# Performance work log

Hardware: AMD Instinct MI355X
Metric: run time of the kernel (lower is better)

The kernel has to match this reference:

```python
import jax, jax.numpy as jnp
import numpy as np
from jax import lax

N_CLS = 3
ALPHA = 2
NMS = True


def _make_level(key, B, A, D, H, W, P, counts):
    k1, k2, k3, k4, k5 = jax.random.split(key, 5)
    C = N_CLS * A
    logit = jax.random.normal(k1, (B, C, D, H, W), dtype=jnp.float32)
    # valid positive coords use d,h,w >= 1 so padded writes to (0,0,0,0) never collide
    a = jax.random.randint(k2, (B, P), 0, A)
    d = jax.random.randint(k3, (B, P), 1, D)
    h = jax.random.randint(k4, (B, P), 1, H)
    w = jax.random.randint(k5, (B, P), 1, W)
    labels = jax.random.randint(jax.random.fold_in(key, 7), (B, P), 0, N_CLS)
    valid = jnp.arange(P)[None, :] < jnp.asarray(counts)[:, None]  # [B,P]
    coord = jnp.stack([a, d, h, w], axis=-1)
    coord = jnp.where(valid[..., None], coord, -1).astype(jnp.int32)
    # ground-truth prob map: -1 = negative, class id (float) at positive voxels
    prob_gt = -jnp.ones((B, A, D, H, W), dtype=jnp.float32)
    cs = jnp.where(valid[..., None], coord, 0)
    b_idx = jnp.arange(B)[:, None]
    vals = jnp.where(valid, labels.astype(jnp.float32), -1.0)
    prob_gt = prob_gt.at[b_idx, cs[..., 0], cs[..., 1], cs[..., 2], cs[..., 3]].set(vals)
    return logit, prob_gt, coord


def setup_inputs() -> dict:
    key = jax.random.key(0)
    kA, kB = jax.random.split(key)
    logit0, prob_gt0, coord0 = _make_level(kA, 4, 3, 64, 64, 64, 128, [128, 64, 32, 0])
    logit1, prob_gt1, coord1 = _make_level(kB, 4, 3, 32, 32, 32, 128, [64, 16, 8, 128])
    weight_cls = jnp.array([1.0, 1.5, 2.0], dtype=jnp.float32)
    return {
        "logit0": logit0, "logit1": logit1,
        "prob_gt0": prob_gt0, "prob_gt1": prob_gt1,
        "coord0": coord0, "coord1": coord1,
        "weight_cls": weight_cls,
    }


def _level_loss(logit, prob_gt, coord_gt, weight_cls):
    B, C, D, H, W = logit.shape
    A = C // N_CLS
    logit = logit.reshape(B, N_CLS, A, D, H, W)
    logp = jax.nn.log_softmax(logit, axis=1)
    nll = -logp                      # [B,N_cls,A,D,H,W]
    prob = jnp.exp(logp)
    nll_neg = nll[:, 0]              # [B,A,D,H,W]
    prob_neg = prob[:, 0]
    negmask = (prob_gt == -1).astype(logit.dtype)
    if NMS:
        mp = lax.reduce_window(nll_neg, -jnp.inf, lax.max,
                               (1, 1, 3, 3, 3), (1, 1, 1, 1, 1),
                               [(0, 0), (0, 0), (1, 1), (1, 1), (1, 1)])
        negmask = negmask * lax.stop_gradient((mp == nll_neg).astype(logit.dtype))
    w_neg = (1.0 - lax.stop_gradient(prob_neg)) ** ALPHA * negmask
    loss_neg = jnp.sum(nll_neg * w_neg)
    count_neg = jnp.sum(w_neg)
    # positives: ragged coord gather, masked instead of per-sample python loop
    valid = coord_gt[:, :, 0] > -1                       # [B,P]
    c = jnp.where(valid[..., None], coord_gt, 0)         # safe coords
    a, d, h, w = c[..., 0], c[..., 1], c[..., 2], c[..., 3]
    b_idx = jnp.arange(B)[:, None]
    cls = prob_gt[b_idx, a, d, h, w].astype(jnp.int32)   # class id at positives
    cls = jnp.where(valid, cls, 0)
    p_t = prob[b_idx, cls, a, d, h, w]
    nll_t = nll[b_idx, cls, a, d, h, w]
    w_pos = ((1.0 - lax.stop_gradient(p_t)) ** ALPHA
             * weight_cls[cls] * valid.astype(logit.dtype))
    loss_pos = jnp.sum(nll_t * w_pos)
    count_pos = jnp.sum(w_pos)
    return loss_pos, loss_neg, count_pos, count_neg


def reference(logit0, logit1, prob_gt0, prob_gt1, coord0, coord1, weight_cls):
    lp0, ln0, cp0, cn0 = _level_loss(logit0, prob_gt0, coord0, weight_cls)
    lp1, ln1, cp1, cn1 = _level_loss(logit1, prob_gt1, coord1, weight_cls)
    return jnp.stack([lp0 + lp1, ln0 + ln1, cp0 + cp1, cn0 + cn1])
```

## Files before the change

### kernel.cpp

```cpp
#include <hip/hip_runtime.h>
#include <math.h>

#define NEG_INF (-INFINITY)

__device__ __forceinline__ float nll3(float l0, float l1, float l2) {
    float m = fmaxf(l0, fmaxf(l1, l2));
    float e0 = __expf(l0 - m);
    float e1 = __expf(l1 - m);
    float e2 = __expf(l2 - m);
    return __logf(e0 + e1 + e2) - (l0 - m);
}

template<int W, int NR, int TD, int D, int H>
__device__ void neg_strip_p2(int uid, int lane,
                             const float* __restrict__ logit,
                             const float* __restrict__ pg,
                             float2* __restrict__ slot) {
    constexpr int LR = W / 4;
    constexpr int NI = NR + 2;
    constexpr int HG = H / NR;
    constexpr int DT = D / TD;
    const int q = lane % LR;
    const int g = lane / LR;

    int t = uid;
    const int hg = t % HG; t /= HG;
    const int dt = t % DT; t /= DT;
    const int ba = t;
    const int a = ba % 3, b = ba / 3;
    const int h0 = hg * NR, d0 = dt * TD;
    const int HW = H * W;

    const long S = (long)D * HW;
    const float* lb  = logit + ((long)b * 9 + a) * S;
    const long  cs   = 3 * S;
    const float* pgb = pg + (long)ba * S;

    const int jrow = h0 - 1 + g;
    const bool hv = (jrow >= 0) && (jrow < H) && (g < NI);
    const int hcl = min(max(jrow, 0), H - 1);
    const int rowoff = hcl * W + 4 * q;
    const int prowoff = (h0 + min(g, NR - 1)) * W + 4 * q;

    float4 A0, A1, A2, B0, B1, B2, C0, C1, C2;
    float4 GA, GB, GC;
    bool vA, vB, vC;

    {
        const float* p = lb + (long)max(d0 - 1, 0) * HW + rowoff;
        A0 = *(const float4*)p;
        A1 = *(const float4*)(p + cs);
        A2 = *(const float4*)(p + 2 * cs);
        vA = (d0 - 1 >= 0);
        const float* p2 = lb + (long)d0 * HW + rowoff;
        B0 = *(const float4*)p2;
        B1 = *(const float4*)(p2 + cs);
        B2 = *(const float4*)(p2 + 2 * cs);
        vB = true;
        GA = make_float4(0.f, 0.f, 0.f, 0.f);
        GB = make_float4(0.f, 0.f, 0.f, 0.f);
    }

    float vm0[4], vm1[4], cc1[4];
#pragma unroll
    for (int i = 0; i < 4; ++i) { vm0[i] = NEG_INF; vm1[i] = NEG_INF; cc1[i] = 0.f; }

    float loss = 0.f, cnt = 0.f;

#pragma unroll
    for (int s = 0; s <= TD + 1; ++s) {
        if (s <= TD - 1) {
            const int pd = d0 + 1 + s;
            const float* p = lb + (long)min(pd, D - 1) * HW + rowoff;
            C0 = *(const float4*)p;
            C1 = *(const float4*)(p + cs);
            C2 = *(const float4*)(p + 2 * cs);
            vC = (pd < D);
            GC = *(const float4*)(pgb + (long)(d0 + s) * HW + prowoff);
        } else {
            vC = false;
            C0 = C1 = C2 = make_float4(0.f, 0.f, 0.f, 0.f);
            GC = make_float4(0.f, 0.f, 0.f, 0.f);
        }

        float nvv[4];
        {
            const bool vv = vA && hv;
            nvv[0] = vv ? nll3(A0.x, A1.x, A2.x) : NEG_INF;
            nvv[1] = vv ? nll3(A0.y, A1.y, A2.y) : NEG_INF;
            nvv[2] = vv ? nll3(A0.z, A1.z, A2.z) : NEG_INF;
            nvv[3] = vv ? nll3(A0.w, A1.w, A2.w) : NEG_INF;
        }

        float le = __shfl(nvv[3], lane - 1);
        float re = __shfl(nvv[0], lane + 1);
        le = (q == 0)      ? NEG_INF : le;
        re = (q == LR - 1) ? NEG_INF : re;
        float rm[4];
        rm[0] = fmaxf(le,     fmaxf(nvv[0], nvv[1]));
        rm[1] = fmaxf(nvv[0], fmaxf(nvv[1], nvv[2]));
        rm[2] = fmaxf(nvv[1], fmaxf(nvv[2], nvv[3]));
        rm[3] = fmaxf(nvv[2], fmaxf(nvv[3], re));

        float rmA[4], rmB[4], ctr[4];
#pragma unroll
        for (int i = 0; i < 4; ++i) {
            rmA[i] = __shfl(rm[i],  lane + LR);
            rmB[i] = __shfl(rm[i],  lane + 2 * LR);
            ctr[i] = __shfl(nvv[i], lane + LR);
        }

        const float pgv[4] = {GA.x, GA.y, GA.z, GA.w};
#pragma unroll
        for (int i = 0; i < 4; ++i) {
            float hw2 = fmaxf(rm[i], fmaxf(rmA[i], rmB[i]));
            if (s >= 2 && g < NR && pgv[i] == -1.0f) {
                float mp = fmaxf(vm0[i], fmaxf(vm1[i], hw2));
                if (mp == cc1[i]) {
                    float pn = __expf(-cc1[i]);
                    float wn = (1.f - pn) * (1.f - pn);
                    loss += cc1[i] * wn;
                    cnt  += wn;
                }
            }
            vm0[i] = vm1[i]; vm1[i] = hw2; cc1[i] = ctr[i];
        }

        GA = GB; GB = GC;
        A0 = B0; A1 = B1; A2 = B2; vA = vB;
        B0 = C0; B1 = C1; B2 = C2; vB = vC;
    }

#pragma unroll
    for (int off = 32; off > 0; off >>= 1) {
        loss += __shfl_down(loss, off);
        cnt  += __shfl_down(cnt, off);
    }
    if (lane == 0) slot[uid] = make_float2(loss, cnt);
}

__device__ void pos_wave8(int sub, int lane,
                          const float* __restrict__ logit,
                          const float* __restrict__ prob_gt,
                          const int* __restrict__ coord,
                          const float* __restrict__ wcls,
                          float2* __restrict__ slot,
                          int D, int H, int W) {
    const int A = 3, P = 128;
    const long S = (long)D * H * W;
    const int i = sub * 64 + lane;
    const int b = i / P;
    const int* c = coord + (long)i * 4;
    const int a = c[0];
    float loss = 0.f, cnt = 0.f;
    if (a > -1) {
        const int d = c[1], h = c[2], w = c[3];
        const long s = ((long)d * H + h) * W + w;
        const int cls = (int)prob_gt[((long)b * A + a) * S + s];
        const float* lp = logit + ((long)b * 3 * A + a) * S + s;
        float l0 = lp[0];
        float l1 = lp[(long)A * S];
        float l2 = lp[2L * A * S];
        float m = fmaxf(l0, fmaxf(l1, l2));
        float e0 = __expf(l0 - m);
        float e1 = __expf(l1 - m);
        float e2 = __expf(l2 - m);
        float lsum = __logf(e0 + e1 + e2);
        float lc = (cls == 0) ? l0 : ((cls == 1) ? l1 : l2);
        float lpc = (lc - m) - lsum;
        float pt = __expf(lpc);
        float wp = (1.f - pt) * (1.f - pt) * wcls[cls];
        loss = (-lpc) * wp;
        cnt = wp;
    }
#pragma unroll
    for (int off = 32; off > 0; off >>= 1) {
        loss += __shfl_down(loss, off);
        cnt  += __shfl_down(cnt, off);
    }
    if (lane == 0) *slot = make_float2(loss, cnt);
}

#define NW0 6144
#define NW1 768
#define NWP 16
#define NUNEG (NW0 + NW1)
#define TOTAL_WAVES (NW0 + NW1 + NWP)

__global__ __launch_bounds__(256)
void mega_kernel(const float* __restrict__ logit0,
                 const float* __restrict__ logit1,
                 const float* __restrict__ pg0,
                 const float* __restrict__ pg1,
                 const int* __restrict__ coord0,
                 const int* __restrict__ coord1,
                 const float* __restrict__ wcls,
                 float2* __restrict__ ws) {
    const int gw = blockIdx.x * 4 + (threadIdx.x >> 6);
    const int lane = threadIdx.x & 63;
    float2* wsneg = ws;
    float2* wspos = ws + NUNEG;
    if (gw < NW0) {
        neg_strip_p2<64, 2, 4, 64, 64>(gw, lane, logit0, pg0, wsneg);
    } else if (gw < NW0 + NW1) {
        neg_strip_p2<32, 4, 4, 32, 32>(gw - NW0, lane, logit1, pg1, wsneg + NW0);
    } else if (gw < NW0 + NW1 + 8) {
        const int sub = gw - NW0 - NW1;
        pos_wave8(sub, lane, logit0, pg0, coord0, wcls, wspos + sub, 64, 64, 64);
    } else {
        const int sub = gw - NW0 - NW1 - 8;
        pos_wave8(sub, lane, logit1, pg1, coord1, wcls, wspos + 8 + sub, 32, 32, 32);
    }
}

__global__ __launch_bounds__(1024)
void final_reduce(const float2* __restrict__ ws, float* __restrict__ out) {
    const float2* wsneg = ws;
    const float2* wspos = ws + NUNEG;
    float ln = 0.f, cn = 0.f, lp = 0.f, cp = 0.f;
    for (int i = threadIdx.x; i < NUNEG; i += 1024) {
        float2 v = wsneg[i]; ln += v.x; cn += v.y;
    }
    if (threadIdx.x < NWP) {
        float2 v = wspos[threadIdx.x]; lp = v.x; cp = v.y;
    }
#pragma unroll
    for (int off = 32; off > 0; off >>= 1) {
        ln += __shfl_down(ln, off); cn += __shfl_down(cn, off);
        lp += __shfl_down(lp, off); cp += __shfl_down(cp, off);
    }
    __shared__ float s[16][4];
    const int wv = threadIdx.x >> 6;
    if ((threadIdx.x & 63) == 0) {
        s[wv][0] = ln; s[wv][1] = cn; s[wv][2] = lp; s[wv][3] = cp;
    }
    __syncthreads();
    if (threadIdx.x == 0) {
        float a = 0.f, b = 0.f, c = 0.f, d = 0.f;
#pragma unroll
        for (int i = 0; i < 16; ++i) {
            a += s[i][0]; b += s[i][1]; c += s[i][2]; d += s[i][3];
        }
        out[0] = c;
        out[1] = a;
        out[2] = d;
        out[3] = b;
    }
}

extern "C" void kernel_launch(void* const* d_in, const int* in_sizes, int n_in,
                              void* d_out, int out_size, void* d_ws, size_t ws_size,
                              hipStream_t stream) {
    const float* logit0   = (const float*)d_in[0];
    const float* logit1   = (const float*)d_in[1];
    const float* prob_gt0 = (const float*)d_in[2];
    const float* prob_gt1 = (const float*)d_in[3];
    const int*   coord0   = (const int*)d_in[4];
    const int*   coord1   = (const int*)d_in[5];
    const float* wcls     = (const float*)d_in[6];
    float* out = (float*)d_out;
    float2* ws = (float2*)d_ws;

    mega_kernel<<<TOTAL_WAVES / 4, 256, 0, stream>>>(
        logit0, logit1, prob_gt0, prob_gt1, coord0, coord1, wcls, ws);
    final_reduce<<<1, 1024, 0, stream>>>(ws, out);
}
```

Measured before the change: 107.7 us.

## Tile negative NMS over whole blocks with LDS-shared NLL and halo reuse

Replaces per-wave 3D max-pool strips with per-block tiles of many H rows. Each block computes NLL once into LDS ring buffers and builds the separable 3x3x3 max from shared row and plane maxima. This cuts the redundant halo loads and NLL recomputation of the small per-wave strips. In exchange it adds LDS traffic, two block barriers per depth step, and an intra-block reduction.

```diff
diff --git a/kernel.cpp b/kernel.cpp
--- a/kernel.cpp
+++ b/kernel.cpp
@@ -11,124 +11,155 @@
     return __logf(e0 + e1 + e2) - (l0 - m);
 }
 
-template<int W, int NR, int TD, int D, int H>
-__device__ void neg_strip_p2(int uid, int lane,
-                             const float* __restrict__ logit,
-                             const float* __restrict__ pg,
-                             float2* __restrict__ slot) {
-    constexpr int LR = W / 4;
-    constexpr int NI = NR + 2;
-    constexpr int HG = H / NR;
-    constexpr int DT = D / TD;
-    const int q = lane % LR;
-    const int g = lane / LR;
-
-    int t = uid;
-    const int hg = t % HG; t /= HG;
-    const int dt = t % DT; t /= DT;
+__device__ __forceinline__ float4 fmax4(float4 a, float4 b) {
+    return make_float4(fmaxf(a.x, b.x), fmaxf(a.y, b.y),
+                       fmaxf(a.z, b.z), fmaxf(a.w, b.w));
+}
+
+template<int W, int HT, int ZT, int D, int H>
+__device__ void neg_block(int ub, int tid,
+                          const float* __restrict__ logit,
+                          const float* __restrict__ pg,
+                          float2* __restrict__ slot,
+                          float* lds, float2* red) {
+    constexpr int LQ = W / 4;
+    constexpr int SR = W + 4;
+    constexpr int SROWS = HT + 2;
+    constexpr int QS = SROWS * LQ;
+    constexpr int HW = H * W;
+    constexpr int ZTI = D / ZT;
+    constexpr int HTI = H / HT;
+    constexpr int NLL_SZ = SROWS * SR;
+    constexpr int HV_OFF = 3 * NLL_SZ;
+    constexpr int HV_SZ = HT * SR;
+
+    int t = ub;
+    const int ht = t % HTI; t /= HTI;
+    const int zt = t % ZTI; t /= ZTI;
     const int ba = t;
     const int a = ba % 3, b = ba / 3;
-    const int h0 = hg * NR, d0 = dt * TD;
-    const int HW = H * W;
+    const int z0 = zt * ZT, h0 = ht * HT;
 
     const long S = (long)D * HW;
+    const long cs = 3 * S;
     const float* lb  = logit + ((long)b * 9 + a) * S;
-    const long  cs   = 3 * S;
     const float* pgb = pg + (long)ba * S;
 
-    const int jrow = h0 - 1 + g;
-    const bool hv = (jrow >= 0) && (jrow < H) && (g < NI);
-    const int hcl = min(max(jrow, 0), H - 1);
-    const int rowoff = hcl * W + 4 * q;
-    const int prowoff = (h0 + min(g, NR - 1)) * W + 4 * q;
-
-    float4 A0, A1, A2, B0, B1, B2, C0, C1, C2;
-    float4 GA, GB, GC;
-    bool vA, vB, vC;
-
-    {
-        const float* p = lb + (long)max(d0 - 1, 0) * HW + rowoff;
-        A0 = *(const float4*)p;
-        A1 = *(const float4*)(p + cs);
-        A2 = *(const float4*)(p + 2 * cs);
-        vA = (d0 - 1 >= 0);
-        const float* p2 = lb + (long)d0 * HW + rowoff;
-        B0 = *(const float4*)p2;
-        B1 = *(const float4*)(p2 + cs);
-        B2 = *(const float4*)(p2 + 2 * cs);
-        vB = true;
-        GA = make_float4(0.f, 0.f, 0.f, 0.f);
-        GB = make_float4(0.f, 0.f, 0.f, 0.f);
-    }
-
-    float vm0[4], vm1[4], cc1[4];
-#pragma unroll
-    for (int i = 0; i < 4; ++i) { vm0[i] = NEG_INF; vm1[i] = NEG_INF; cc1[i] = 0.f; }
+    const int er = tid / LQ;
+    const int q  = tid % LQ;
+    const int lane = tid & 63;
+    const int l_er = er * SR + 4 * q;
+    const int po = (h0 + er) * W + 4 * q;
+
+    int roff[2]; bool rok[2];
+#pragma unroll
+    for (int r = 0; r < 2; ++r) {
+        const int k = tid + 256 * r;
+        const int row = k / LQ, qq = k % LQ;
+        const int h = h0 - 1 + row;
+        rok[r]  = (k < QS) && (h >= 0) && (h < H);
+        roff[r] = min(max(h, 0), H - 1) * W + 4 * qq;
+    }
+
+    float4 rA[2][3] = {}, rB[2][3] = {};
+    float4 pgA = {}, pgB = {};
+    bool pvA, pvB = false;
+
+    auto issue = [&](float4 (&rg)[2][3], int zp) -> bool {
+        const bool pv = (zp >= 0) && (zp < D);
+        if (pv) {
+#pragma unroll
+            for (int r = 0; r < 2; ++r) {
+                if (tid + 256 * r < QS) {
+                    const float* p = lb + (long)zp * HW + roff[r];
+                    rg[r][0] = *(const float4*)p;
+                    rg[r][1] = *(const float4*)(p + cs);
+                    rg[r][2] = *(const float4*)(p + 2 * cs);
+                }
+            }
+        }
+        return pv;
+    };
+
+    pvA = issue(rA, z0 - 1);
 
     float loss = 0.f, cnt = 0.f;
 
 #pragma unroll
-    for (int s = 0; s <= TD + 1; ++s) {
-        if (s <= TD - 1) {
-            const int pd = d0 + 1 + s;
-            const float* p = lb + (long)min(pd, D - 1) * HW + rowoff;
-            C0 = *(const float4*)p;
-            C1 = *(const float4*)(p + cs);
-            C2 = *(const float4*)(p + 2 * cs);
-            vC = (pd < D);
-            GC = *(const float4*)(pgb + (long)(d0 + s) * HW + prowoff);
-        } else {
-            vC = false;
-            C0 = C1 = C2 = make_float4(0.f, 0.f, 0.f, 0.f);
-            GC = make_float4(0.f, 0.f, 0.f, 0.f);
-        }
-
-        float nvv[4];
+    for (int zi = 0; zi <= ZT + 1; ++zi) {
+        const int zc = z0 - 1 + zi;
+        if (zi <= ZT) pvB = issue(rB, zc + 1);
+        if (zi >= 1 && zi <= ZT)
+            pgB = *(const float4*)(pgb + (long)zc * HW + po);
+
         {
-            const bool vv = vA && hv;
-            nvv[0] = vv ? nll3(A0.x, A1.x, A2.x) : NEG_INF;
-            nvv[1] = vv ? nll3(A0.y, A1.y, A2.y) : NEG_INF;
-            nvv[2] = vv ? nll3(A0.z, A1.z, A2.z) : NEG_INF;
-            nvv[3] = vv ? nll3(A0.w, A1.w, A2.w) : NEG_INF;
-        }
-
-        float le = __shfl(nvv[3], lane - 1);
-        float re = __shfl(nvv[0], lane + 1);
-        le = (q == 0)      ? NEG_INF : le;
-        re = (q == LR - 1) ? NEG_INF : re;
-        float rm[4];
-        rm[0] = fmaxf(le,     fmaxf(nvv[0], nvv[1]));
-        rm[1] = fmaxf(nvv[0], fmaxf(nvv[1], nvv[2]));
-        rm[2] = fmaxf(nvv[1], fmaxf(nvv[2], nvv[3]));
-        rm[3] = fmaxf(nvv[2], fmaxf(nvv[3], re));
-
-        float rmA[4], rmB[4], ctr[4];
-#pragma unroll
-        for (int i = 0; i < 4; ++i) {
-            rmA[i] = __shfl(rm[i],  lane + LR);
-            rmB[i] = __shfl(rm[i],  lane + 2 * LR);
-            ctr[i] = __shfl(nvv[i], lane + LR);
-        }
-
-        const float pgv[4] = {GA.x, GA.y, GA.z, GA.w};
-#pragma unroll
-        for (int i = 0; i < 4; ++i) {
-            float hw2 = fmaxf(rm[i], fmaxf(rmA[i], rmB[i]));
-            if (s >= 2 && g < NR && pgv[i] == -1.0f) {
-                float mp = fmaxf(vm0[i], fmaxf(vm1[i], hw2));
-                if (mp == cc1[i]) {
-                    float pn = __expf(-cc1[i]);
+            float* nb = lds + (zi % 3) * NLL_SZ;
+#pragma unroll
+            for (int r = 0; r < 2; ++r) {
+                const int k = tid + 256 * r;
+                if (k < QS) {
+                    const int row = k / LQ, qq = k % LQ;
+                    const bool ok = pvA && rok[r];
+                    float4 n;
+                    n.x = ok ? nll3(rA[r][0].x, rA[r][1].x, rA[r][2].x) : NEG_INF;
+                    n.y = ok ? nll3(rA[r][0].y, rA[r][1].y, rA[r][2].y) : NEG_INF;
+                    n.z = ok ? nll3(rA[r][0].z, rA[r][1].z, rA[r][2].z) : NEG_INF;
+                    n.w = ok ? nll3(rA[r][0].w, rA[r][1].w, rA[r][2].w) : NEG_INF;
+                    *(float4*)(nb + row * SR + 4 * qq) = n;
+                }
+            }
+        }
+        __syncthreads();
+
+        {
+            const float* nb = lds + (zi % 3) * NLL_SZ;
+            float* hb = lds + HV_OFF + (zi % 3) * HV_SZ;
+            float4 v0 = *(const float4*)(nb + l_er);
+            float4 v1 = *(const float4*)(nb + l_er + SR);
+            float4 v2 = *(const float4*)(nb + l_er + 2 * SR);
+            float4 vm = fmax4(v0, fmax4(v1, v2));
+            float le = __shfl(vm.w, lane - 1);
+            float re = __shfl(vm.x, lane + 1);
+            le = (q == 0)      ? NEG_INF : le;
+            re = (q == LQ - 1) ? NEG_INF : re;
+            float4 hv;
+            hv.x = fmaxf(le,   fmaxf(vm.x, vm.y));
+            hv.y = fmaxf(vm.x, fmaxf(vm.y, vm.z));
+            hv.z = fmaxf(vm.y, fmaxf(vm.z, vm.w));
+            hv.w = fmaxf(vm.z, fmaxf(vm.w, re));
+            *(float4*)(hb + l_er) = hv;
+        }
+        __syncthreads();
+
+        if (zi >= 2) {
+            const float* nbm = lds + ((zi - 1) % 3) * NLL_SZ;
+            const float* hb0 = lds + HV_OFF + ((zi - 2) % 3) * HV_SZ;
+            const float* hb1 = lds + HV_OFF + ((zi - 1) % 3) * HV_SZ;
+            const float* hb2 = lds + HV_OFF + (zi % 3) * HV_SZ;
+            float4 nc = *(const float4*)(nbm + l_er + SR);
+            float4 m  = fmax4(*(const float4*)(hb0 + l_er),
+                        fmax4(*(const float4*)(hb1 + l_er),
+                              *(const float4*)(hb2 + l_er)));
+            const float pgv[4] = {pgA.x, pgA.y, pgA.z, pgA.w};
+            const float ncv[4] = {nc.x, nc.y, nc.z, nc.w};
+            const float mv[4]  = {m.x, m.y, m.z, m.w};
+#pragma unroll
+            for (int i = 0; i < 4; ++i) {
+                if (pgv[i] == -1.0f && mv[i] == ncv[i]) {
+                    float pn = __expf(-ncv[i]);
                     float wn = (1.f - pn) * (1.f - pn);
-                    loss += cc1[i] * wn;
+                    loss += ncv[i] * wn;
                     cnt  += wn;
                 }
             }
-            vm0[i] = vm1[i]; vm1[i] = hw2; cc1[i] = ctr[i];
-        }
-
-        GA = GB; GB = GC;
-        A0 = B0; A1 = B1; A2 = B2; vA = vB;
-        B0 = C0; B1 = C1; B2 = C2; vB = vC;
+        }
+
+        pvA = pvB;
+#pragma unroll
+        for (int r = 0; r < 2; ++r)
+#pragma unroll
+            for (int c = 0; c < 3; ++c) rA[r][c] = rB[r][c];
+        pgA = pgB;
     }
 
 #pragma unroll
@@ -136,7 +167,14 @@
         loss += __shfl_down(loss, off);
         cnt  += __shfl_down(cnt, off);
     }
-    if (lane == 0) slot[uid] = make_float2(loss, cnt);
+    if (lane == 0) red[tid >> 6] = make_float2(loss, cnt);
+    __syncthreads();
+    if (tid == 0) {
+        float sx = 0.f, sy = 0.f;
+#pragma unroll
+        for (int i = 0; i < 4; ++i) { sx += red[i].x; sy += red[i].y; }
+        *slot = make_float2(sx, sy);
+    }
 }
 
 __device__ void pos_wave8(int sub, int lane,
@@ -181,11 +219,12 @@
     if (lane == 0) *slot = make_float2(loss, cnt);
 }
 
-#define NW0 6144
-#define NW1 768
+#define NB0 768
+#define NB1 96
+#define NBNEG (NB0 + NB1)
+#define NBP 4
+#define TOTAL_BLOCKS (NBNEG + NBP)
 #define NWP 16
-#define NUNEG (NW0 + NW1)
-#define TOTAL_WAVES (NW0 + NW1 + NWP)
 
 __global__ __launch_bounds__(256)
 void mega_kernel(const float* __restrict__ logit0,
@@ -196,29 +235,32 @@
                  const int* __restrict__ coord1,
                  const float* __restrict__ wcls,
                  float2* __restrict__ ws) {
-    const int gw = blockIdx.x * 4 + (threadIdx.x >> 6);
-    const int lane = threadIdx.x & 63;
+    __shared__ float lds[7128];
+    __shared__ float2 red[4];
+    const int bid = blockIdx.x;
+    const int tid = threadIdx.x;
     float2* wsneg = ws;
-    float2* wspos = ws + NUNEG;
-    if (gw < NW0) {
-        neg_strip_p2<64, 2, 4, 64, 64>(gw, lane, logit0, pg0, wsneg);
-    } else if (gw < NW0 + NW1) {
-        neg_strip_p2<32, 4, 4, 32, 32>(gw - NW0, lane, logit1, pg1, wsneg + NW0);
-    } else if (gw < NW0 + NW1 + 8) {
-        const int sub = gw - NW0 - NW1;
-        pos_wave8(sub, lane, logit0, pg0, coord0, wcls, wspos + sub, 64, 64, 64);
+    float2* wspos = ws + NBNEG;
+    if (bid < NB0) {
+        neg_block<64, 16, 4, 64, 64>(bid, tid, logit0, pg0, wsneg + bid, lds, red);
+    } else if (bid < NBNEG) {
+        neg_block<32, 32, 4, 32, 32>(bid - NB0, tid, logit1, pg1, wsneg + bid, lds, red);
     } else {
-        const int sub = gw - NW0 - NW1 - 8;
-        pos_wave8(sub, lane, logit1, pg1, coord1, wcls, wspos + 8 + sub, 32, 32, 32);
+        const int gwl = (bid - NBNEG) * 4 + (tid >> 6);
+        const int lane = tid & 63;
+        if (gwl < 8)
+            pos_wave8(gwl, lane, logit0, pg0, coord0, wcls, wspos + gwl, 64, 64, 64);
+        else
+            pos_wave8(gwl - 8, lane, logit1, pg1, coord1, wcls, wspos + gwl, 32, 32, 32);
     }
 }
 
 __global__ __launch_bounds__(1024)
 void final_reduce(const float2* __restrict__ ws, float* __restrict__ out) {
     const float2* wsneg = ws;
-    const float2* wspos = ws + NUNEG;
+    const float2* wspos = ws + NBNEG;
     float ln = 0.f, cn = 0.f, lp = 0.f, cp = 0.f;
-    for (int i = threadIdx.x; i < NUNEG; i += 1024) {
+    for (int i = threadIdx.x; i < NBNEG; i += 1024) {
         float2 v = wsneg[i]; ln += v.x; cn += v.y;
     }
     if (threadIdx.x < NWP) {
@@ -261,7 +303,7 @@
     float* out = (float*)d_out;
     float2* ws = (float2*)d_ws;
 
-    mega_kernel<<<TOTAL_WAVES / 4, 256, 0, stream>>>(
+    mega_kernel<<<TOTAL_BLOCKS, 256, 0, stream>>>(
         logit0, logit1, prob_gt0, prob_gt1, coord0, coord1, wcls, ws);
     final_reduce<<<1, 1024, 0, stream>>>(ws, out);
 }
```

Result: faster. 105.3 us (-2.2%).
